# Optimization experiments

Measured on AMD Instinct MI355X. Metric: run time of the kernel, lower is better.

Reference implementation:

```python
import jax, jax.numpy as jnp
import numpy as np

INIT_RANGE = 0.02

def setup_inputs() -> dict:
    key = jax.random.key(0)
    ks = jax.random.split(key, 5)
    B, S, D, H, Dh = 4, 2048, 768, 12, 64
    residual = jax.random.normal(ks[0], (B, S, D), dtype=jnp.float32)
    W_Q = jax.random.normal(ks[1], (H, D, Dh), dtype=jnp.float32) * INIT_RANGE
    W_K = jax.random.normal(ks[2], (H, D, Dh), dtype=jnp.float32) * INIT_RANGE
    W_V = jax.random.normal(ks[3], (H, D, Dh), dtype=jnp.float32) * INIT_RANGE
    W_O = jax.random.normal(ks[4], (H, Dh, D), dtype=jnp.float32) * INIT_RANGE
    b_Q = jnp.zeros((H, Dh), dtype=jnp.float32)
    b_K = jnp.zeros((H, Dh), dtype=jnp.float32)
    b_V = jnp.zeros((H, Dh), dtype=jnp.float32)
    b_O = jnp.zeros((D,), dtype=jnp.float32)
    return {"residual": residual, "W_Q": W_Q, "W_K": W_K, "W_V": W_V,
            "W_O": W_O, "b_Q": b_Q, "b_K": b_K, "b_V": b_V, "b_O": b_O}

def reference(residual, W_Q, W_K, W_V, W_O, b_Q, b_K, b_V, b_O):
    # residual: [b, s, d]; W_{Q,K,V}: [h, d, dh]; W_O: [h, dh, d]
    d_head = W_Q.shape[-1]
    q = jnp.einsum('bsd,hde->bshe', residual, W_Q) + b_Q  # [b, s, h, dh]
    k = jnp.einsum('bsd,hde->bshe', residual, W_K) + b_K
    v = jnp.einsum('bsd,hde->bshe', residual, W_V) + b_V
    scores = jnp.einsum('bqhe,bkhe->bhqk', q, k) / jnp.sqrt(jnp.float32(d_head))
    S = residual.shape[1]
    causal = jnp.tril(jnp.ones((S, S), dtype=bool))  # True where attending allowed
    scores = jnp.where(causal, scores, -jnp.inf)
    pattern = jax.nn.softmax(scores, axis=-1)  # [b, h, q, k]
    z = jnp.einsum('bkhe,bhqk->bqhe', v, pattern)  # [b, q, h, dh]
    attn_out = jnp.einsum('bqhe,hed->bqd', z, W_O) + b_O
    return attn_out
```

## Files before the change

kernel.cpp:

```cpp
#include <hip/hip_runtime.h>

typedef short short8 __attribute__((ext_vector_type(8)));
typedef float floatx4 __attribute__((ext_vector_type(4)));
typedef unsigned short ushort_t;


__device__ inline ushort_t f2bf(float f) {
  union { float f; unsigned u; } x; x.f = f;
  unsigned u = x.u;
  unsigned r = u + 0x7fffu + ((u >> 16) & 1u);
  return (ushort_t)(r >> 16);
}

__device__ inline unsigned cvtpk(float a, float b) {
  unsigned r;
  asm("v_cvt_pk_bf16_f32 %0, %1, %2" : "=v"(r) : "v"(a), "v"(b));
  return r;
}

__device__ inline float fexp2(float x) {
#if __has_builtin(__builtin_amdgcn_exp2f)
  return __builtin_amdgcn_exp2f(x);
#else
  return exp2f(x);
#endif
}

__device__ inline void async16(const void* g, void* l) {
  __builtin_amdgcn_global_load_lds((const __attribute__((address_space(1))) void*)g,
                                   (__attribute__((address_space(3))) void*)l,
                                   16, 0, 0);
}


__global__ __launch_bounds__(256) void conv_prep(
    const float* __restrict__ x, ushort_t* __restrict__ rx,
    const float* __restrict__ wq, const float* __restrict__ wk, const float* __restrict__ wv,
    const float* __restrict__ wo,
    const float* __restrict__ bq, const float* __restrict__ bk, const float* __restrict__ bv,
    ushort_t* __restrict__ wqkvT, ushort_t* __restrict__ woT, float* __restrict__ bqkv)
{
  __shared__ ushort_t t[64 * 72];
  const int tid = threadIdx.x;
  const int bid0 = blockIdx.x;
  if (bid0 < 6144) {
    int i = bid0 * 256 + tid;
    float4 f = ((const float4*)x)[i];
    ushort4 o;
    o.x = f2bf(f.x); o.y = f2bf(f.y); o.z = f2bf(f.z); o.w = f2bf(f.w);
    ((ushort4*)rx)[i] = o;
    return;
  }
  const int bid = bid0 - 6144;
  if (bid < 432) {
    int m = bid / 144, rem = bid % 144;
    int h = rem / 12, dt = rem % 12;
    int d0 = dt * 64;
    const float* w = (m == 0) ? wq : ((m == 1) ? wk : wv);
    const float* src = w + ((size_t)h * 768 + d0) * 64;
#pragma unroll
    for (int i = 0; i < 4; ++i) {
      int task = i * 256 + tid;
      int row = task >> 4, c4 = task & 15;
      float4 f = *(const float4*)(src + row * 64 + c4 * 4);
      ushort4 o4;
      o4.x = f2bf(f.x); o4.y = f2bf(f.y); o4.z = f2bf(f.z); o4.w = f2bf(f.w);
      *(ushort4*)&t[row * 72 + c4 * 4] = o4;
    }
    __syncthreads();
    ushort_t* dst = wqkvT + ((size_t)m * 768 + h * 64) * 768 + d0;
#pragma unroll
    for (int i = 0; i < 2; ++i) {
      int task = i * 256 + tid;
      int e = task >> 3, sc = task & 7;
      short8 d8;
#pragma unroll
      for (int j = 0; j < 8; ++j) d8[j] = (short)t[(sc * 8 + j) * 72 + e];
      *(short8*)(dst + (size_t)e * 768 + sc * 8) = d8;
    }
  } else if (bid < 576) {
    int b2 = bid - 432;
    int het = b2 / 12, dt = b2 % 12;
    int he0 = het * 64, d0 = dt * 64;
    const float* src = wo + (size_t)he0 * 768 + d0;
#pragma unroll
    for (int i = 0; i < 4; ++i) {
      int task = i * 256 + tid;
      int row = task >> 4, c4 = task & 15;
      float4 f = *(const float4*)(src + (size_t)row * 768 + c4 * 4);
      ushort4 o4;
      o4.x = f2bf(f.x); o4.y = f2bf(f.y); o4.z = f2bf(f.z); o4.w = f2bf(f.w);
      *(ushort4*)&t[row * 72 + c4 * 4] = o4;
    }
    __syncthreads();
    ushort_t* dst = woT + (size_t)d0 * 768 + he0;
#pragma unroll
    for (int i = 0; i < 2; ++i) {
      int task = i * 256 + tid;
      int dd = task >> 3, sc = task & 7;
      short8 d8;
#pragma unroll
      for (int j = 0; j < 8; ++j) d8[j] = (short)t[(sc * 8 + j) * 72 + dd];
      *(short8*)(dst + (size_t)dd * 768 + sc * 8) = d8;
    }
  } else {
    for (int idx = tid; idx < 2304; idx += 256) {
      int m = idx / 768, rem = idx - m * 768;
      const float* bp = (m == 0) ? bq : ((m == 1) ? bk : bv);
      bqkv[idx] = bp[rem];
    }
  }
}


__global__ __launch_bounds__(256) void gemm_qkv(
    const ushort_t* __restrict__ A, const ushort_t* __restrict__ Bt,
    const float* __restrict__ bias,
    ushort_t* __restrict__ q, ushort_t* __restrict__ k, ushort_t* __restrict__ vt)
{
  __shared__ __align__(16) ushort_t sh[32768];
  const int tid = threadIdx.x;
  const int wave = tid >> 6, lane = tid & 63;
  const int ln15 = lane & 15, quad = lane >> 4;
  const int id = blockIdx.x;
  const int xk = id & 7, j = id >> 3;
  const int bx = (xk >> 1) * 16 + (j & 15);
  const int by = (xk & 1) * 9 + (j >> 4);
  const int row0 = bx * 128, col0 = by * 128;
  const int wm = (wave >> 1) * 64, wn = (wave & 1) * 64;

  const int sr = tid >> 3;
  const int sc = (tid & 7) ^ (sr & 7);
  const ushort_t* gA0 = A + (size_t)(row0 + sr) * 768 + sc * 8;
  const ushort_t* gB0 = Bt + (size_t)(col0 + sr) * 768 + sc * 8;

  const int l7 = ln15 & 7;
  const int baA = (wm + ln15) * 64;
  const int baB = (wn + ln15) * 64;
  const int sl0 = (quad ^ l7) * 8;
  const int sl1 = ((quad + 4) ^ l7) * 8;

  floatx4 acc[4][4];
#pragma unroll
  for (int mi = 0; mi < 4; ++mi)
#pragma unroll
    for (int ni = 0; ni < 4; ++ni)
      acc[mi][ni] = (floatx4){0.f, 0.f, 0.f, 0.f};

#pragma unroll
  for (int i = 0; i < 4; ++i) {
    async16(gA0 + i * 32 * 768, &sh[(i * 256 + tid) * 8]);
    async16(gB0 + i * 32 * 768, &sh[16384 + (i * 256 + tid) * 8]);
  }
  __syncthreads();

  for (int kt = 0; kt < 12; ++kt) {
    const int buf = kt & 1;
    if (kt + 1 < 12) {
      ushort_t* dA = &sh[(buf ^ 1) * 8192];
      ushort_t* dB = &sh[16384 + (buf ^ 1) * 8192];
      const ushort_t* ga = gA0 + (kt + 1) * 64;
      const ushort_t* gb = gB0 + (kt + 1) * 64;
#pragma unroll
      for (int i = 0; i < 4; ++i) {
        async16(ga + i * 32 * 768, dA + (i * 256 + tid) * 8);
        async16(gb + i * 32 * 768, dB + (i * 256 + tid) * 8);
      }
    }
    const ushort_t* sA = &sh[buf * 8192];
    const ushort_t* sB = &sh[16384 + buf * 8192];
    short8 af[4][2], bfv[4][2];
#pragma unroll
    for (int mi = 0; mi < 4; ++mi) {
      af[mi][0] = *(const short8*)&sA[baA + mi * 1024 + sl0];
      af[mi][1] = *(const short8*)&sA[baA + mi * 1024 + sl1];
    }
#pragma unroll
    for (int ni = 0; ni < 4; ++ni) {
      bfv[ni][0] = *(const short8*)&sB[baB + ni * 1024 + sl0];
      bfv[ni][1] = *(const short8*)&sB[baB + ni * 1024 + sl1];
    }
#pragma unroll
    for (int mi = 0; mi < 4; ++mi)
#pragma unroll
      for (int ni = 0; ni < 4; ++ni) {
        acc[mi][ni] = __builtin_amdgcn_mfma_f32_16x16x32_bf16(af[mi][0], bfv[ni][0], acc[mi][ni], 0, 0, 0);
        acc[mi][ni] = __builtin_amdgcn_mfma_f32_16x16x32_bf16(af[mi][1], bfv[ni][1], acc[mi][ni], 0, 0, 0);
      }
    __syncthreads();
  }

  if (col0 < 1536) {
    const float qscale = 0.125f * 1.44269504f;
#pragma unroll
    for (int mi = 0; mi < 4; ++mi) {
#pragma unroll
      for (int ni = 0; ni < 4; ++ni) {
        int gr = row0 + wm + mi * 16 + quad * 4;
        int gc = col0 + wn + ni * 16 + ln15;
        float bia = bias[gc];
        int m = gc / 768;
        int rem = gc - m * 768;
        int h = rem >> 6, e = rem & 63;
        ushort_t* dp = (m == 0) ? q : k;
#pragma unroll
        for (int r = 0; r < 4; ++r) {
          float val = acc[mi][ni][r] + bia;
          int rr = gr + r;
          int bb = rr >> 11, ss = rr & 2047;
          size_t dst = ((size_t)((bb * 12 + h) * 2048 + ss) << 6) + e;
          dp[dst] = f2bf((m == 0) ? val * qscale : val);
        }
      }
    }
  } else {
#pragma unroll
    for (int mi = 0; mi < 4; ++mi) {
#pragma unroll
      for (int ni = 0; ni < 4; ++ni) {
        int col = wn + ni * 16 + ln15;
        int rowb = wm + mi * 16 + quad * 4;
        int rowc = rowb >> 2;
        int msw = (col & 7) << 2;
        float bia = bias[col0 + col];
        ushort4 w4;
        w4.x = f2bf(acc[mi][ni][0] + bia);
        w4.y = f2bf(acc[mi][ni][1] + bia);
        w4.z = f2bf(acc[mi][ni][2] + bia);
        w4.w = f2bf(acc[mi][ni][3] + bia);
        *(ushort4*)&sh[col * 128 + ((rowc ^ msw) << 2)] = w4;
      }
    }
    __syncthreads();
    const int relc0 = col0 - 1536;
    const int bb = row0 >> 11, s0 = row0 & 2047;
#pragma unroll
    for (int i = 0; i < 8; ++i) {
      int g = i * 256 + tid;
      int col = g >> 4, chunk = g & 15;
      int msw = (col & 7) << 2;
      short8 d = *(const short8*)&sh[col * 128 + (((chunk * 2) ^ msw) << 2)];
      int hh = (relc0 + col) >> 6;
      int ee = col & 63;
      *(short8*)(vt + (((size_t)(bb * 12 + hh) * 64 + ee) << 11) + s0 + chunk * 8) = d;
    }
  }
}


__global__ __launch_bounds__(256) void gemm_out(
    const ushort_t* __restrict__ A, const ushort_t* __restrict__ Bt,
    const float* __restrict__ bias, float* __restrict__ outf)
{
  __shared__ __align__(16) ushort_t sh[24576];
  const int tid = threadIdx.x;
  const int wave = tid >> 6, lane = tid & 63;
  const int ln15 = lane & 15, quad = lane >> 4;
  const int id = blockIdx.x;
  const int xk = id & 7, j = id >> 3;
  const int bx = xk * 16 + (j & 15);
  const int by = j >> 4;
  const int row0 = bx * 64, col0 = by * 128;
  const int wm = (wave >> 1) * 32, wn = (wave & 1) * 64;

  const int sr = tid >> 3;
  const int sc = (tid & 7) ^ (sr & 7);
  const ushort_t* gA0 = A + (size_t)(row0 + sr) * 768 + sc * 8;
  const ushort_t* gB0 = Bt + (size_t)(col0 + sr) * 768 + sc * 8;

  const int l7 = ln15 & 7;
  const int baA = (wm + ln15) * 64;
  const int baB = (wn + ln15) * 64;
  const int sl0 = (quad ^ l7) * 8;
  const int sl1 = ((quad + 4) ^ l7) * 8;

  floatx4 acc[2][4];
#pragma unroll
  for (int mi = 0; mi < 2; ++mi)
#pragma unroll
    for (int ni = 0; ni < 4; ++ni)
      acc[mi][ni] = (floatx4){0.f, 0.f, 0.f, 0.f};

#pragma unroll
  for (int i = 0; i < 2; ++i)
    async16(gA0 + i * 32 * 768, &sh[(i * 256 + tid) * 8]);
#pragma unroll
  for (int i = 0; i < 4; ++i)
    async16(gB0 + i * 32 * 768, &sh[8192 + (i * 256 + tid) * 8]);
  __syncthreads();

  for (int kt = 0; kt < 12; ++kt) {
    const int buf = kt & 1;
    if (kt + 1 < 12) {
      ushort_t* dA = &sh[(buf ^ 1) * 4096];
      ushort_t* dB = &sh[8192 + (buf ^ 1) * 8192];
      const ushort_t* ga = gA0 + (kt + 1) * 64;
      const ushort_t* gb = gB0 + (kt + 1) * 64;
#pragma unroll
      for (int i = 0; i < 2; ++i)
        async16(ga + i * 32 * 768, dA + (i * 256 + tid) * 8);
#pragma unroll
      for (int i = 0; i < 4; ++i)
        async16(gb + i * 32 * 768, dB + (i * 256 + tid) * 8);
    }
    const ushort_t* sA = &sh[buf * 4096];
    const ushort_t* sB = &sh[8192 + buf * 8192];
    short8 af[2][2], bfv[4][2];
#pragma unroll
    for (int mi = 0; mi < 2; ++mi) {
      af[mi][0] = *(const short8*)&sA[baA + mi * 1024 + sl0];
      af[mi][1] = *(const short8*)&sA[baA + mi * 1024 + sl1];
    }
#pragma unroll
    for (int ni = 0; ni < 4; ++ni) {
      bfv[ni][0] = *(const short8*)&sB[baB + ni * 1024 + sl0];
      bfv[ni][1] = *(const short8*)&sB[baB + ni * 1024 + sl1];
    }
#pragma unroll
    for (int mi = 0; mi < 2; ++mi)
#pragma unroll
      for (int ni = 0; ni < 4; ++ni) {
        acc[mi][ni] = __builtin_amdgcn_mfma_f32_16x16x32_bf16(af[mi][0], bfv[ni][0], acc[mi][ni], 0, 0, 0);
        acc[mi][ni] = __builtin_amdgcn_mfma_f32_16x16x32_bf16(af[mi][1], bfv[ni][1], acc[mi][ni], 0, 0, 0);
      }
    __syncthreads();
  }

#pragma unroll
  for (int mi = 0; mi < 2; ++mi) {
#pragma unroll
    for (int ni = 0; ni < 4; ++ni) {
      int gr = row0 + wm + mi * 16 + quad * 4;
      int gc = col0 + wn + ni * 16 + ln15;
      float bia = bias[gc];
#pragma unroll
      for (int r = 0; r < 4; ++r)
        outf[(size_t)(gr + r) * 768 + gc] = acc[mi][ni][r] + bia;
    }
  }
}


__device__ inline short8 frag_ld(const ushort_t* t, int row, int ch) {
  return *(const short8*)&t[row * 64 + (((ch ^ row) & 7) * 8)];
}

__global__ __launch_bounds__(256) void attn3(
    const ushort_t* __restrict__ Q, const ushort_t* __restrict__ K,
    const ushort_t* __restrict__ VT, ushort_t* __restrict__ Z)
{
  __shared__ ushort_t lK[2][64 * 64];
  __shared__ ushort_t lV[2][64 * 64];
  const int tid = threadIdx.x;
  const int wave = tid >> 6, lane = tid & 63;
  const int ln15 = lane & 15, quad = lane >> 4;
  const int bi = blockIdx.x;
  const int bh = bi % 48;
  const int t = 15 - (bi / 48);
  const int h = bh % 12, b = bh / 12;
  const size_t base = (size_t)bh * 2048 * 64;
  const ushort_t* Qp = Q + base + (size_t)t * 128 * 64;
  const ushort_t* Kp = K + base;
  const ushort_t* Vp = VT + base;
  const int nk = 2 * t + 2;

  const int srow = tid >> 3, slch = tid & 7;
  const int sc_ = slch ^ (srow & 7);
  const int krow = (srow & 3) | ((srow & 0x0C) << 1) | ((srow & 0x10) >> 2);

  short8 qf[2][2];
#pragma unroll
  for (int c = 0; c < 2; ++c) {
    const ushort_t* qr = Qp + (wave * 32 + c * 16 + ln15) * 64 + quad * 8;
    qf[c][0] = *(const short8*)qr;
    qf[c][1] = *(const short8*)(qr + 32);
  }

  async16(Kp + (size_t)krow * 64 + sc_ * 8, &lK[0][tid * 8]);
  async16(Kp + (size_t)(krow + 32) * 64 + sc_ * 8, &lK[0][(256 + tid) * 8]);
  async16(Vp + (size_t)srow * 2048 + sc_ * 8, &lV[0][tid * 8]);
  async16(Vp + (size_t)(srow + 32) * 2048 + sc_ * 8, &lV[0][(256 + tid) * 8]);

  const ushort_t* kPre0 = Kp + (size_t)(64 + krow) * 64 + sc_ * 8;
  const ushort_t* kPre1 = kPre0 + 32 * 64;
  const ushort_t* vPre0 = Vp + (size_t)srow * 2048 + 64 + sc_ * 8;
  const ushort_t* vPre1 = vPre0 + 32 * 2048;

  __syncthreads();

  float l_i[2] = {0.f, 0.f};
  floatx4 o[2][4];
#pragma unroll
  for (int c = 0; c < 2; ++c)
#pragma unroll
    for (int et = 0; et < 4; ++et) o[c][et] = (floatx4){0.f, 0.f, 0.f, 0.f};

  const int qg0 = t * 128 + wave * 32 + ln15;

  for (int kt = 0; kt < nk; ++kt) {
    const int buf = kt & 1;
    if (kt + 1 < nk) {
      ushort_t* dK = lK[buf ^ 1];
      ushort_t* dV = lV[buf ^ 1];
      async16(kPre0, dK + tid * 8);
      async16(kPre1, dK + (256 + tid) * 8);
      async16(vPre0, dV + tid * 8);
      async16(vPre1, dV + (256 + tid) * 8);
      kPre0 += 4096; kPre1 += 4096; vPre0 += 64; vPre1 += 64;
    }

    floatx4 st[2][4];
#pragma unroll
    for (int ni = 0; ni < 4; ++ni) {
      short8 kf0 = frag_ld(lK[buf], ni * 16 + ln15, quad);
      short8 kf1 = frag_ld(lK[buf], ni * 16 + ln15, quad + 4);
#pragma unroll
      for (int c = 0; c < 2; ++c) {
        floatx4 z4 = (floatx4){0.f, 0.f, 0.f, 0.f};
        z4 = __builtin_amdgcn_mfma_f32_16x16x32_bf16(kf0, qf[c][0], z4, 0, 0, 0);
        st[c][ni] = __builtin_amdgcn_mfma_f32_16x16x32_bf16(kf1, qf[c][1], z4, 0, 0, 0);
      }
    }

    const bool masked = (kt >= 2 * t);
    short8 pf[2][2];
#pragma unroll
    for (int c = 0; c < 2; ++c) {
      const int qg = qg0 + c * 16;
      float p[16];
      float rs = 0.f;
#pragma unroll
      for (int ni = 0; ni < 4; ++ni) {
#pragma unroll
        for (int r = 0; r < 4; ++r) {
          float x = st[c][ni][r];
          if (masked) {
            int kg = kt * 64 + (ni >> 1) * 32 + quad * 8 + (ni & 1) * 4 + r;
            x = (kg <= qg) ? x : -1e30f;
          }
          p[ni * 4 + r] = fexp2(x);
        }
        rs += (p[ni * 4 + 0] + p[ni * 4 + 1]) + (p[ni * 4 + 2] + p[ni * 4 + 3]);
      }
      rs += __shfl_xor(rs, 16);
      rs += __shfl_xor(rs, 32);
      l_i[c] += rs;
      union { unsigned u[4]; short8 s8; } w0, w1;
#pragma unroll
      for (int i2 = 0; i2 < 4; ++i2) {
        w0.u[i2] = cvtpk(p[i2 * 2], p[i2 * 2 + 1]);
        w1.u[i2] = cvtpk(p[8 + i2 * 2], p[8 + i2 * 2 + 1]);
      }
      pf[c][0] = w0.s8;
      pf[c][1] = w1.s8;
    }

#pragma unroll
    for (int et = 0; et < 4; ++et) {
      short8 vf0 = frag_ld(lV[buf], et * 16 + ln15, quad);
      short8 vf1 = frag_ld(lV[buf], et * 16 + ln15, quad + 4);
#pragma unroll
      for (int c = 0; c < 2; ++c) {
        o[c][et] = __builtin_amdgcn_mfma_f32_16x16x32_bf16(vf0, pf[c][0], o[c][et], 0, 0, 0);
        o[c][et] = __builtin_amdgcn_mfma_f32_16x16x32_bf16(vf1, pf[c][1], o[c][et], 0, 0, 0);
      }
    }
    __syncthreads();
  }

#pragma unroll
  for (int c = 0; c < 2; ++c) {
    float inv = 1.f / l_i[c];
    size_t zrow = (size_t)(b * 2048 + t * 128 + wave * 32 + c * 16 + ln15);
#pragma unroll
    for (int et = 0; et < 4; ++et) {
      ushort4 w;
      w.x = f2bf(o[c][et][0] * inv);
      w.y = f2bf(o[c][et][1] * inv);
      w.z = f2bf(o[c][et][2] * inv);
      w.w = f2bf(o[c][et][3] * inv);
      *(ushort4*)&Z[zrow * 768 + h * 64 + et * 16 + quad * 4] = w;
    }
  }
}


extern "C" void kernel_launch(void* const* d_in, const int* in_sizes, int n_in,
                              void* d_out, int out_size, void* d_ws, size_t ws_size,
                              hipStream_t stream)
{
  const float* residual = (const float*)d_in[0];
  const float* W_Q = (const float*)d_in[1];
  const float* W_K = (const float*)d_in[2];
  const float* W_V = (const float*)d_in[3];
  const float* W_O = (const float*)d_in[4];
  const float* b_Q = (const float*)d_in[5];
  const float* b_K = (const float*)d_in[6];
  const float* b_V = (const float*)d_in[7];
  const float* b_O = (const float*)d_in[8];
  float* out = (float*)d_out;

  char* w = (char*)d_ws;
  ushort_t* rx    = (ushort_t*)(w + 0);
  ushort_t* wqkvT = (ushort_t*)(w + 12582912);
  ushort_t* woT   = (ushort_t*)(w + 16121856);
  float*    bqkv  = (float*)   (w + 17301504);
  ushort_t* q     = (ushort_t*)(w + 17310720);
  ushort_t* k     = (ushort_t*)(w + 29893632);
  ushort_t* vt    = (ushort_t*)(w + 55059456);
  ushort_t* z     = rx;

  conv_prep<<<6721, 256, 0, stream>>>(residual, rx, W_Q, W_K, W_V, W_O,
                                      b_Q, b_K, b_V, wqkvT, woT, bqkv);
  gemm_qkv<<<1152, 256, 0, stream>>>(rx, wqkvT, bqkv, q, k, vt);
  attn3<<<768, 256, 0, stream>>>(q, k, vt, z);
  gemm_out<<<768, 256, 0, stream>>>(z, woT, b_O, out);
}
```

Baseline: 200.9 us.

## Process two K/V tiles per barrier and skip fully masked subtiles per wave

The attention loop now stages 128 keys (two 64-key subtiles) per double-buffered iteration, which halves the number of __syncthreads and loop iterations. Each wave computes only the subtiles up to its own causal limit and skips subtiles that would be entirely masked. Only the final subtile for each wave gets the per-element mask. In exchange, LDS usage doubles, which may lower occupancy, and waves in a block now do uneven amounts of work.

```diff
diff --git a/kernel.cpp b/kernel.cpp
--- a/kernel.cpp
+++ b/kernel.cpp
@@ -349,8 +349,8 @@
     const ushort_t* __restrict__ Q, const ushort_t* __restrict__ K,
     const ushort_t* __restrict__ VT, ushort_t* __restrict__ Z)
 {
-  __shared__ ushort_t lK[2][64 * 64];
-  __shared__ ushort_t lV[2][64 * 64];
+  __shared__ ushort_t lK[2][2 * 64 * 64];
+  __shared__ ushort_t lV[2][2][64 * 64];
   const int tid = threadIdx.x;
   const int wave = tid >> 6, lane = tid & 63;
   const int ln15 = lane & 15, quad = lane >> 4;
@@ -362,7 +362,8 @@
   const ushort_t* Qp = Q + base + (size_t)t * 128 * 64;
   const ushort_t* Kp = K + base;
   const ushort_t* Vp = VT + base;
-  const int nk = 2 * t + 2;
+  const int nt = t + 1;
+  const int lasts = 2 * t + (wave >> 1);
 
   const int srow = tid >> 3, slch = tid & 7;
   const int sc_ = slch ^ (srow & 7);
@@ -376,14 +377,18 @@
     qf[c][1] = *(const short8*)(qr + 32);
   }
 
-  async16(Kp + (size_t)krow * 64 + sc_ * 8, &lK[0][tid * 8]);
+  async16(Kp + (size_t)krow * 64 + sc_ * 8,        &lK[0][tid * 8]);
   async16(Kp + (size_t)(krow + 32) * 64 + sc_ * 8, &lK[0][(256 + tid) * 8]);
-  async16(Vp + (size_t)srow * 2048 + sc_ * 8, &lV[0][tid * 8]);
-  async16(Vp + (size_t)(srow + 32) * 2048 + sc_ * 8, &lV[0][(256 + tid) * 8]);
-
-  const ushort_t* kPre0 = Kp + (size_t)(64 + krow) * 64 + sc_ * 8;
+  async16(Kp + (size_t)(krow + 64) * 64 + sc_ * 8, &lK[0][4096 + tid * 8]);
+  async16(Kp + (size_t)(krow + 96) * 64 + sc_ * 8, &lK[0][4096 + (256 + tid) * 8]);
+  async16(Vp + (size_t)srow * 2048 + sc_ * 8,             &lV[0][0][tid * 8]);
+  async16(Vp + (size_t)(srow + 32) * 2048 + sc_ * 8,      &lV[0][0][(256 + tid) * 8]);
+  async16(Vp + (size_t)srow * 2048 + 64 + sc_ * 8,        &lV[0][1][tid * 8]);
+  async16(Vp + (size_t)(srow + 32) * 2048 + 64 + sc_ * 8, &lV[0][1][(256 + tid) * 8]);
+
+  const ushort_t* kPre0 = Kp + (size_t)(128 + krow) * 64 + sc_ * 8;
   const ushort_t* kPre1 = kPre0 + 32 * 64;
-  const ushort_t* vPre0 = Vp + (size_t)srow * 2048 + 64 + sc_ * 8;
+  const ushort_t* vPre0 = Vp + (size_t)srow * 2048 + 128 + sc_ * 8;
   const ushort_t* vPre1 = vPre0 + 32 * 2048;
 
   __syncthreads();
@@ -397,72 +402,86 @@
 
   const int qg0 = t * 128 + wave * 32 + ln15;
 
-  for (int kt = 0; kt < nk; ++kt) {
+  for (int kt = 0; kt < nt; ++kt) {
     const int buf = kt & 1;
-    if (kt + 1 < nk) {
+    if (kt + 1 < nt) {
       ushort_t* dK = lK[buf ^ 1];
-      ushort_t* dV = lV[buf ^ 1];
-      async16(kPre0, dK + tid * 8);
-      async16(kPre1, dK + (256 + tid) * 8);
-      async16(vPre0, dV + tid * 8);
-      async16(vPre1, dV + (256 + tid) * 8);
-      kPre0 += 4096; kPre1 += 4096; vPre0 += 64; vPre1 += 64;
-    }
-
-    floatx4 st[2][4];
-#pragma unroll
-    for (int ni = 0; ni < 4; ++ni) {
-      short8 kf0 = frag_ld(lK[buf], ni * 16 + ln15, quad);
-      short8 kf1 = frag_ld(lK[buf], ni * 16 + ln15, quad + 4);
-#pragma unroll
-      for (int c = 0; c < 2; ++c) {
-        floatx4 z4 = (floatx4){0.f, 0.f, 0.f, 0.f};
-        z4 = __builtin_amdgcn_mfma_f32_16x16x32_bf16(kf0, qf[c][0], z4, 0, 0, 0);
-        st[c][ni] = __builtin_amdgcn_mfma_f32_16x16x32_bf16(kf1, qf[c][1], z4, 0, 0, 0);
-      }
-    }
-
-    const bool masked = (kt >= 2 * t);
-    short8 pf[2][2];
-#pragma unroll
-    for (int c = 0; c < 2; ++c) {
-      const int qg = qg0 + c * 16;
-      float p[16];
-      float rs = 0.f;
-#pragma unroll
-      for (int ni = 0; ni < 4; ++ni) {
-#pragma unroll
-        for (int r = 0; r < 4; ++r) {
-          float x = st[c][ni][r];
-          if (masked) {
-            int kg = kt * 64 + (ni >> 1) * 32 + quad * 8 + (ni & 1) * 4 + r;
-            x = (kg <= qg) ? x : -1e30f;
+      ushort_t* dV0 = lV[buf ^ 1][0];
+      ushort_t* dV1 = lV[buf ^ 1][1];
+      async16(kPre0,        dK + tid * 8);
+      async16(kPre1,        dK + (256 + tid) * 8);
+      async16(kPre0 + 4096, dK + 4096 + tid * 8);
+      async16(kPre1 + 4096, dK + 4096 + (256 + tid) * 8);
+      async16(vPre0,        dV0 + tid * 8);
+      async16(vPre1,        dV0 + (256 + tid) * 8);
+      async16(vPre0 + 64,   dV1 + tid * 8);
+      async16(vPre1 + 64,   dV1 + (256 + tid) * 8);
+      kPre0 += 8192; kPre1 += 8192; vPre0 += 128; vPre1 += 128;
+    }
+
+#pragma unroll
+    for (int h2 = 0; h2 < 2; ++h2) {
+      const int s = 2 * kt + h2;
+      if (s <= lasts) {
+        const ushort_t* lKh = &lK[buf][h2 * 4096];
+        const ushort_t* lVh = lV[buf][h2];
+
+        floatx4 st[2][4];
+#pragma unroll
+        for (int ni = 0; ni < 4; ++ni) {
+          short8 kf0 = frag_ld(lKh, ni * 16 + ln15, quad);
+          short8 kf1 = frag_ld(lKh, ni * 16 + ln15, quad + 4);
+#pragma unroll
+          for (int c = 0; c < 2; ++c) {
+            floatx4 z4 = (floatx4){0.f, 0.f, 0.f, 0.f};
+            z4 = __builtin_amdgcn_mfma_f32_16x16x32_bf16(kf0, qf[c][0], z4, 0, 0, 0);
+            st[c][ni] = __builtin_amdgcn_mfma_f32_16x16x32_bf16(kf1, qf[c][1], z4, 0, 0, 0);
           }
-          p[ni * 4 + r] = fexp2(x);
         }
-        rs += (p[ni * 4 + 0] + p[ni * 4 + 1]) + (p[ni * 4 + 2] + p[ni * 4 + 3]);
-      }
-      rs += __shfl_xor(rs, 16);
-      rs += __shfl_xor(rs, 32);
-      l_i[c] += rs;
-      union { unsigned u[4]; short8 s8; } w0, w1;
-#pragma unroll
-      for (int i2 = 0; i2 < 4; ++i2) {
-        w0.u[i2] = cvtpk(p[i2 * 2], p[i2 * 2 + 1]);
-        w1.u[i2] = cvtpk(p[8 + i2 * 2], p[8 + i2 * 2 + 1]);
-      }
-      pf[c][0] = w0.s8;
-      pf[c][1] = w1.s8;
-    }
-
-#pragma unroll
-    for (int et = 0; et < 4; ++et) {
-      short8 vf0 = frag_ld(lV[buf], et * 16 + ln15, quad);
-      short8 vf1 = frag_ld(lV[buf], et * 16 + ln15, quad + 4);
-#pragma unroll
-      for (int c = 0; c < 2; ++c) {
-        o[c][et] = __builtin_amdgcn_mfma_f32_16x16x32_bf16(vf0, pf[c][0], o[c][et], 0, 0, 0);
-        o[c][et] = __builtin_amdgcn_mfma_f32_16x16x32_bf16(vf1, pf[c][1], o[c][et], 0, 0, 0);
+
+        const bool masked = (s == lasts);
+        short8 pf[2][2];
+#pragma unroll
+        for (int c = 0; c < 2; ++c) {
+          const int qg = qg0 + c * 16;
+          float p[16];
+          float rs = 0.f;
+#pragma unroll
+          for (int ni = 0; ni < 4; ++ni) {
+#pragma unroll
+            for (int r = 0; r < 4; ++r) {
+              float x = st[c][ni][r];
+              if (masked) {
+                int kg = s * 64 + (ni >> 1) * 32 + quad * 8 + (ni & 1) * 4 + r;
+                x = (kg <= qg) ? x : -1e30f;
+              }
+              p[ni * 4 + r] = fexp2(x);
+            }
+            rs += (p[ni * 4 + 0] + p[ni * 4 + 1]) + (p[ni * 4 + 2] + p[ni * 4 + 3]);
+          }
+          rs += __shfl_xor(rs, 16);
+          rs += __shfl_xor(rs, 32);
+          l_i[c] += rs;
+          union { unsigned u[4]; short8 s8; } w0, w1;
+#pragma unroll
+          for (int i2 = 0; i2 < 4; ++i2) {
+            w0.u[i2] = cvtpk(p[i2 * 2], p[i2 * 2 + 1]);
+            w1.u[i2] = cvtpk(p[8 + i2 * 2], p[8 + i2 * 2 + 1]);
+          }
+          pf[c][0] = w0.s8;
+          pf[c][1] = w1.s8;
+        }
+
+#pragma unroll
+        for (int et = 0; et < 4; ++et) {
+          short8 vf0 = frag_ld(lVh, et * 16 + ln15, quad);
+          short8 vf1 = frag_ld(lVh, et * 16 + ln15, quad + 4);
+#pragma unroll
+          for (int c = 0; c < 2; ++c) {
+            o[c][et] = __builtin_amdgcn_mfma_f32_16x16x32_bf16(vf0, pf[c][0], o[c][et], 0, 0, 0);
+            o[c][et] = __builtin_amdgcn_mfma_f32_16x16x32_bf16(vf1, pf[c][1], o[c][et], 0, 0, 0);
+          }
+        }
       }
     }
     __syncthreads();
```

New measurement: 197.3 us. About the same (-1.8%).
